# Optimization experiments

Hardware: AMD Instinct MI355X
Metric: run time of the kernel (lower is better)

The kernel has to match this reference:

```python
import math
import jax, jax.numpy as jnp
import numpy as np

NUM_HEADS = 32
HIDDEN = 4096
HEAD_DIM = HIDDEN // NUM_HEADS  # 128
NEG_INF = -1e30


def _alibi_slopes(n: int) -> jnp.ndarray:
    cp2 = 2 ** math.floor(math.log2(n))
    base = 2.0 ** (-(2.0 ** (-(math.log2(cp2) - 3))))
    slopes = base ** np.arange(1, cp2 + 1, dtype=np.float64)
    if cp2 != n:
        extra_base = 2.0 ** (-(2.0 ** (-(math.log2(2 * cp2) - 3))))
        rem = min(cp2, n - cp2)
        extra = extra_base ** np.arange(1, 1 + 2 * rem, 2, dtype=np.float64)
        slopes = np.concatenate([slopes, extra])
    return jnp.asarray(slopes, dtype=jnp.float32)


def setup_inputs() -> dict:
    key = jax.random.key(0)
    k1, k2, k3 = jax.random.split(key, 3)
    B, S = 2, 2048
    hidden_states = jax.random.normal(k1, (B, S, HIDDEN), dtype=jnp.float32)
    Wqkv = jax.random.normal(k2, (HIDDEN, NUM_HEADS * HEAD_DIM + 2 * HEAD_DIM), dtype=jnp.float32) * 0.02
    Wo = jax.random.normal(k3, (HIDDEN, HIDDEN), dtype=jnp.float32) * 0.02
    return {"hidden_states": hidden_states, "Wqkv": Wqkv, "Wo": Wo}


def reference(hidden_states, Wqkv, Wo):
    B, S, H = hidden_states.shape
    nH, d = NUM_HEADS, HEAD_DIM
    scale = d ** -0.5

    qkv = hidden_states @ Wqkv                      # [B,S,nH*d + 2d]
    q = qkv[..., : nH * d].reshape(B, S, nH, d)     # [B,S,nH,d]
    k = qkv[..., nH * d: nH * d + d]                # [B,S,d] (single kv head, MQA)
    v = qkv[..., nH * d + d:]                       # [B,S,d]

    scores = jnp.einsum("bqhd,bkd->bhqk", q, k) * scale  # [B,nH,S,S]

    pos_q = jnp.arange(S)[:, None]
    pos_k = jnp.arange(S)[None, :]
    slopes = _alibi_slopes(nH)                       # [nH]
    alibi = slopes[:, None, None] * (pos_k - pos_q).astype(jnp.float32)  # [nH,S,S]
    causal = pos_k <= pos_q                          # [S,S]

    scores = jnp.where(causal[None, None], scores + alibi[None], NEG_INF)
    probs = jax.nn.softmax(scores, axis=-1)
    attn = jnp.einsum("bhqk,bkd->bqhd", probs, v).reshape(B, S, H)
    return attn @ Wo
```

## Files before the change

kernel.cpp:

```cpp
#include <hip/hip_runtime.h>
#include <hip/hip_bf16.h>

typedef __attribute__((ext_vector_type(8))) short bf16x8;
typedef __attribute__((ext_vector_type(4))) float f32x4;
typedef __attribute__((ext_vector_type(8))) unsigned short u16x8;
typedef __attribute__((ext_vector_type(4))) unsigned short u16x4;

__device__ __forceinline__ unsigned short f2bf(float x) {
    union { float f; unsigned u; } v; v.f = x;
    unsigned r = v.u + 0x7fff + ((v.u >> 16) & 1);
    return (unsigned short)(r >> 16);
}

__device__ __forceinline__ unsigned short f2bf_hw(float x) {
    __hip_bfloat16 h = __float2bfloat16(x);
    return *reinterpret_cast<unsigned short*>(&h);
}

__device__ __forceinline__ void gload16(const void* g, void* l) {
    __builtin_amdgcn_global_load_lds(
        (const __attribute__((address_space(1))) void*)g,
        (__attribute__((address_space(3))) void*)l, 16, 0, 0);
}

__global__ __launch_bounds__(256) void cast_bf16_kernel(
    const float* __restrict__ src, unsigned short* __restrict__ dst, int n8) {
    int i = blockIdx.x * 256 + threadIdx.x;
    if (i >= n8) return;
    const float4* s = (const float4*)src + (size_t)i * 2;
    float4 a = s[0], b = s[1];
    u16x8 o;
    o[0] = f2bf(a.x); o[1] = f2bf(a.y); o[2] = f2bf(a.z); o[3] = f2bf(a.w);
    o[4] = f2bf(b.x); o[5] = f2bf(b.y); o[6] = f2bf(b.z); o[7] = f2bf(b.w);
    *(u16x8*)(dst + (size_t)i * 8) = o;
}

__global__ __launch_bounds__(256) void transpose_cast_kernel(
    const float* __restrict__ src, unsigned short* __restrict__ dst, int R, int C) {
    __shared__ float tile[32][33];
    const int bx = blockIdx.x * 32, by = blockIdx.y * 32;
    const int tx = threadIdx.x & 31, ty = threadIdx.x >> 5;
#pragma unroll
    for (int i = 0; i < 32; i += 8)
        tile[ty + i][tx] = src[(size_t)(by + ty + i) * C + (bx + tx)];
    __syncthreads();
#pragma unroll
    for (int i = 0; i < 32; i += 8)
        dst[(size_t)(bx + ty + i) * R + (by + tx)] = f2bf(tile[tx][ty + i]);
}

template <int OUTBF>
__global__ __launch_bounds__(256) void gemm_kernel(
    const unsigned short* __restrict__ A, const unsigned short* __restrict__ BT,
    void* __restrict__ Cp, int M, int N, int K) {
    __shared__ unsigned short Al[2][128 * 32];
    __shared__ unsigned short Bl[2][128 * 32];
    const int t = threadIdx.x;
    const int wid = t >> 6, lane = t & 63;
    const int l15 = lane & 15, lg = lane >> 4;
    const int bm = blockIdx.y * 128, bn = blockIdx.x * 128;
    const int wm = (wid >> 1) * 64, wn = (wid & 1) * 64;

    f32x4 acc[4][4];
#pragma unroll
    for (int i = 0; i < 4; ++i)
#pragma unroll
        for (int j = 0; j < 4; ++j) acc[i][j] = (f32x4)(0.f);

    const int nk = K >> 5;
    const int c0 = t, c1 = t + 256;

    auto stage = [&](int buf, int kt) {
        const unsigned short* Ab = A + (size_t)bm * K + kt * 32;
        const unsigned short* Bb = BT + (size_t)bn * K + kt * 32;
        gload16(Ab + (size_t)(c0 >> 2) * K + (c0 & 3) * 8, &Al[buf][wid * 64 * 8]);
        gload16(Ab + (size_t)(c1 >> 2) * K + (c1 & 3) * 8, &Al[buf][(256 + wid * 64) * 8]);
        gload16(Bb + (size_t)(c0 >> 2) * K + (c0 & 3) * 8, &Bl[buf][wid * 64 * 8]);
        gload16(Bb + (size_t)(c1 >> 2) * K + (c1 & 3) * 8, &Bl[buf][(256 + wid * 64) * 8]);
    };

    stage(0, 0);
    __syncthreads();
    for (int kt = 0; kt < nk; ++kt) {
        const int cur = kt & 1;
        if (kt + 1 < nk) stage(cur ^ 1, kt + 1);
        bf16x8 af[4], bfr[4];
#pragma unroll
        for (int i = 0; i < 4; ++i) {
            af[i]  = *(const bf16x8*)&Al[cur][(wm + i * 16 + l15) * 32 + lg * 8];
            bfr[i] = *(const bf16x8*)&Bl[cur][(wn + i * 16 + l15) * 32 + lg * 8];
        }
#pragma unroll
        for (int i = 0; i < 4; ++i)
#pragma unroll
            for (int j = 0; j < 4; ++j)
                acc[i][j] = __builtin_amdgcn_mfma_f32_16x16x32_bf16(af[i], bfr[j], acc[i][j], 0, 0, 0);
        __syncthreads();
    }

#pragma unroll
    for (int i = 0; i < 4; ++i)
#pragma unroll
        for (int j = 0; j < 4; ++j)
#pragma unroll
            for (int r = 0; r < 4; ++r) {
                const int row = bm + wm + i * 16 + lg * 4 + r;
                const int col = bn + wn + j * 16 + l15;
                if (OUTBF) ((unsigned short*)Cp)[(size_t)row * N + col] = f2bf(acc[i][j][r]);
                else       ((float*)Cp)[(size_t)row * N + col] = acc[i][j][r];
            }
}

#define SYNC1() do { __builtin_amdgcn_s_barrier(); \
    asm volatile("s_waitcnt lgkmcnt(0)" ::: "memory"); } while (0)
#define GATE6() do { asm volatile("s_waitcnt vmcnt(6)" ::: "memory"); \
    __builtin_amdgcn_s_barrier(); __builtin_amdgcn_sched_barrier(0); } while (0)

template <int OUTBF>
__global__ __launch_bounds__(512, 2) void gemm256_kernel(
    const unsigned short* __restrict__ A, const unsigned short* __restrict__ BT,
    void* __restrict__ Cp, int K, int N) {
    __shared__ __align__(16) char lds[131072];
    const int t = threadIdx.x;
    const int wid = t >> 6, lane = t & 63;
    const int l15 = lane & 15, lg = lane >> 4;
    const int xcd = blockIdx.x & 7, idx = blockIdx.x >> 3;
    const int bm = ((xcd >> 1) * 4 + (idx >> 3)) * 256;
    const int bn = ((xcd & 1) * 8 + (idx & 7)) * 256;
    const int wmh = wid >> 2;
    const int wq  = wid & 3;
    const int bhf = wq >> 1;
    const int br0 = (wq & 1) * 64;

    auto Ab = [&](int b, int h) -> char* { return lds + ((b * 2 + h) << 14); };
    auto Bb = [&](int b, int h) -> char* { return lds + 65536 + ((b * 2 + h) << 14); };

    auto stage = [&](char* halfBase, const unsigned short* mat, int rowBase, int kt) {
#pragma unroll
        for (int j = 0; j < 2; ++j) {
            const int dbase = ((j << 3) + wid) << 10;
            const int q = (dbase + lane * 16) ^ (lane & 32);
            const int p = q >> 13, r = (q >> 6) & 127, cb = q & 63;
            gload16(mat + (size_t)(rowBase + r) * K + (kt << 6) + (p << 5) + (cb >> 1),
                    halfBase + dbase);
        }
    };

    f32x4 acc[8][4];
#pragma unroll
    for (int i = 0; i < 8; ++i)
#pragma unroll
        for (int j = 0; j < 4; ++j) acc[i][j] = (f32x4)(0.f);

    bf16x8 af[8][2];
    bf16x8 bfr[2][2];

    auto ldA = [&](int b) {
        const char* base = Ab(b, wmh);
#pragma unroll
        for (int i = 0; i < 8; ++i) {
            const int r = i * 16 + l15;
            const int sw = ((r >> 3) & 1) << 5;
#pragma unroll
            for (int kk = 0; kk < 2; ++kk)
                af[i][kk] = *(const bf16x8*)(base + ((kk * 8192 + r * 64 + lg * 16) ^ sw));
        }
    };
    auto ldB = [&](int b, int nh) {
        const char* base = Bb(b, bhf);
#pragma unroll
        for (int i = 0; i < 2; ++i) {
            const int r = br0 + (nh * 2 + i) * 16 + l15;
            const int sw = ((r >> 3) & 1) << 5;
#pragma unroll
            for (int kk = 0; kk < 2; ++kk)
                bfr[i][kk] = *(const bf16x8*)(base + ((kk * 8192 + r * 64 + lg * 16) ^ sw));
        }
    };
    auto MF = [&](int mh, int nh) {
        __builtin_amdgcn_s_setprio(1);
#pragma unroll
        for (int i = 0; i < 4; ++i)
#pragma unroll
            for (int j = 0; j < 2; ++j)
#pragma unroll
                for (int kk = 0; kk < 2; ++kk)
                    acc[mh * 4 + i][nh * 2 + j] = __builtin_amdgcn_mfma_f32_16x16x32_bf16(
                        af[mh * 4 + i][kk], bfr[j][kk], acc[mh * 4 + i][nh * 2 + j], 0, 0, 0);
        __builtin_amdgcn_s_setprio(0);
    };

    stage(Ab(0, 0), A, bm, 0);
    stage(Ab(0, 1), A, bm + 128, 0);
    stage(Bb(0, 0), BT, bn, 0);
    stage(Bb(0, 1), BT, bn + 128, 0);
    stage(Ab(1, 0), A, bm, 1);
    stage(Ab(1, 1), A, bm + 128, 1);
    stage(Bb(1, 0), BT, bn, 1);
    asm volatile("s_waitcnt vmcnt(6)" ::: "memory");
    __builtin_amdgcn_s_barrier();
    __builtin_amdgcn_sched_barrier(0);

    const int kmask = (K >> 6) - 1;
    const int niter = K >> 7;
    for (int it = 0; it < niter; ++it) {
        const int kto = 2 * it + 1;
        const int kne = (2 * it + 2) & kmask;
        const int kno = (2 * it + 3) & kmask;
        ldA(0); ldB(0, 0);
        stage(Bb(1, 1), BT, bn + 128, kto);
        SYNC1(); MF(0, 0); __builtin_amdgcn_s_barrier();
        stage(Ab(0, 0), A, bm, kne);
        SYNC1(); MF(1, 0); __builtin_amdgcn_s_barrier();
        ldB(0, 1);
        stage(Ab(0, 1), A, bm + 128, kne);
        SYNC1(); MF(1, 1); __builtin_amdgcn_s_barrier();
        stage(Bb(0, 0), BT, bn, kne);
        SYNC1(); MF(0, 1); GATE6();
        ldA(1); ldB(1, 0);
        stage(Bb(0, 1), BT, bn + 128, kne);
        SYNC1(); MF(0, 0); __builtin_amdgcn_s_barrier();
        stage(Ab(1, 0), A, bm, kno);
        SYNC1(); MF(1, 0); __builtin_amdgcn_s_barrier();
        ldB(1, 1);
        stage(Ab(1, 1), A, bm + 128, kno);
        SYNC1(); MF(1, 1); __builtin_amdgcn_s_barrier();
        stage(Bb(1, 0), BT, bn, kno);
        SYNC1(); MF(0, 1); GATE6();
    }

#pragma unroll
    for (int mi = 0; mi < 8; ++mi)
#pragma unroll
        for (int ni = 0; ni < 4; ++ni)
#pragma unroll
            for (int rr = 0; rr < 4; ++rr) {
                const size_t off = (size_t)(bm + wmh * 128 + mi * 16 + lg * 4 + rr) * N +
                                   bn + wq * 64 + ni * 16 + l15;
                if (OUTBF) ((unsigned short*)Cp)[off] = f2bf(acc[mi][ni][rr]);
                else       ((float*)Cp)[off] = acc[mi][ni][rr];
            }
}

__global__ __launch_bounds__(256, 4) void attn_kernel(
    const unsigned short* __restrict__ qkv, unsigned short* __restrict__ attn, int S) {
    constexpr int LD = 4352;
    __shared__ unsigned short Kl[64 * 128];
    __shared__ unsigned short Vt[128 * 64];
    __shared__ unsigned short Pl[4][16 * 64];
    const int t = threadIdx.x, wid = t >> 6;
    const int lane = t & 63, l15 = lane & 15, lg = lane >> 4;
    const int h = blockIdx.y, b = blockIdx.z;
    const size_t rb = (size_t)b * S;
    const int nQB = S >> 6;
    const float scale2 = 0.08838834764831845f * 1.4426950408889634f;
    const float slope2 = exp2f(-0.25f * (float)(h + 1)) * 1.4426950408889634f;
    const float sr1 = slope2, sr2 = slope2 * 2.f, sr3 = slope2 * 3.f;

    for (int half = 0; half < 2; ++half) {
        const int qblk = half ? (nQB - 1 - (int)blockIdx.x) : (int)blockIdx.x;
        const int q0w = qblk * 64 + wid * 16;
        const int qlane = q0w + l15;
        const float aq = slope2 * (float)qlane;

        bf16x8 qf[4];
        {
            const unsigned short* qrow = qkv + (rb + qlane) * LD + h * 128 + lg * 8;
#pragma unroll
            for (int j = 0; j < 4; ++j) qf[j] = *(const bf16x8*)(qrow + j * 32);
        }
        f32x4 o[8];
#pragma unroll
        for (int i = 0; i < 8; ++i) o[i] = (f32x4)(0.f);
        float m_ = -1e30f, l_ = 0.f;

        const int ntile = qblk + 1;
        for (int tile = 0; tile < ntile; ++tile) {
            const int t0 = tile * 64;
            {
                const char* kbase = (const char*)(qkv + (rb + t0) * LD + 4096);
#pragma unroll
                for (int i = 0; i < 4; ++i) {
                    const int c = i * 256 + t;
                    const int krow = c >> 4;
                    gload16(kbase + (size_t)krow * (LD * 2) + (((c & 15) * 16) ^ ((krow & 7) << 4)),
                            (char*)Kl + (i * 256 + wid * 64) * 16);
                }
            }
            {
                const unsigned short* vs = qkv + (rb + t0 + lane) * LD + 4224 + wid * 32;
                u16x8 v0 = *(const u16x8*)vs;
                u16x8 v1 = *(const u16x8*)(vs + 8);
                u16x8 v2 = *(const u16x8*)(vs + 16);
                u16x8 v3 = *(const u16x8*)(vs + 24);
                const int kb = 2 * lane;
#pragma unroll
                for (int e = 0; e < 8; ++e) {
                    int dd = wid * 32 + e;
                    *(unsigned short*)((char*)Vt + dd * 128 + (kb ^ ((dd & 7) << 4))) = v0[e];
                    dd += 8;
                    *(unsigned short*)((char*)Vt + dd * 128 + (kb ^ ((dd & 7) << 4))) = v1[e];
                    dd += 8;
                    *(unsigned short*)((char*)Vt + dd * 128 + (kb ^ ((dd & 7) << 4))) = v2[e];
                    dd += 8;
                    *(unsigned short*)((char*)Vt + dd * 128 + (kb ^ ((dd & 7) << 4))) = v3[e];
                }
            }
            __syncthreads();

            f32x4 s4[4];
#pragma unroll
            for (int ct = 0; ct < 4; ++ct) {
                s4[ct] = (f32x4)(0.f);
                const int row = ct * 16 + l15;
                const int swz = (row & 7) << 4;
#pragma unroll
                for (int j = 0; j < 4; ++j) {
                    bf16x8 kf = *(const bf16x8*)((const char*)Kl + row * 256 +
                                                 ((j * 64 + lg * 16) ^ swz));
                    s4[ct] = __builtin_amdgcn_mfma_f32_16x16x32_bf16(kf, qf[j], s4[ct], 0, 0, 0);
                }
            }

            const float base = slope2 * (float)(t0 + lg * 4) - aq;
            float p4[4][4];
            float mx = -1e30f;
            const bool lastt = (tile == ntile - 1);
            const int dbase = t0 + lg * 4 - qlane;
#pragma unroll
            for (int ct = 0; ct < 4; ++ct) {
                const float bbc = base + slope2 * 16.f * (float)ct;
#pragma unroll
                for (int r = 0; r < 4; ++r) {
                    float sc = fmaf(s4[ct][r], scale2,
                                    bbc + (r == 0 ? 0.f : (r == 1 ? sr1 : (r == 2 ? sr2 : sr3))));
                    if (lastt && (dbase + ct * 16 + r > 0)) sc = -1e30f;
                    p4[ct][r] = sc;
                    mx = fmaxf(mx, sc);
                }
            }
            mx = fmaxf(mx, __shfl_xor(mx, 16));
            mx = fmaxf(mx, __shfl_xor(mx, 32));

            if (!__all(mx <= m_ + 8.0f)) {
                const float mnew = fmaxf(m_, mx);
                const float corr = exp2f(m_ - mnew);
                m_ = mnew;
                l_ *= corr;
                float cr[4];
#pragma unroll
                for (int r = 0; r < 4; ++r) cr[r] = __shfl(corr, lg * 4 + r);
#pragma unroll
                for (int n = 0; n < 8; ++n) {
                    o[n][0] *= cr[0]; o[n][1] *= cr[1];
                    o[n][2] *= cr[2]; o[n][3] *= cr[3];
                }
            }

            float rs = 0.f;
#pragma unroll
            for (int ct = 0; ct < 4; ++ct)
#pragma unroll
                for (int r = 0; r < 4; ++r) {
                    const float pv = exp2f(p4[ct][r] - m_);
                    p4[ct][r] = pv;
                    rs += pv;
                }
            rs += __shfl_xor(rs, 16);
            rs += __shfl_xor(rs, 32);
            l_ += rs;

            {
                char* pb = (char*)&Pl[wid][0] + l15 * 128;
                const int swz = (l15 & 7) << 4;
#pragma unroll
                for (int ct = 0; ct < 4; ++ct) {
                    u16x4 w;
                    w[0] = f2bf_hw(p4[ct][0]); w[1] = f2bf_hw(p4[ct][1]);
                    w[2] = f2bf_hw(p4[ct][2]); w[3] = f2bf_hw(p4[ct][3]);
                    *(u16x4*)(pb + ((ct * 32 + lg * 8) ^ swz)) = w;
                }
            }

            const char* pb = (const char*)&Pl[wid][0] + l15 * 128;
            const int pswz = (l15 & 7) << 4;
            bf16x8 pa0 = *(const bf16x8*)(pb + ((lg * 16) ^ pswz));
            bf16x8 pa1 = *(const bf16x8*)(pb + ((64 + lg * 16) ^ pswz));
#pragma unroll
            for (int n = 0; n < 8; ++n) {
                const int dd = n * 16 + l15;
                const int vswz = (dd & 7) << 4;
                bf16x8 vf0 = *(const bf16x8*)((const char*)Vt + dd * 128 + ((lg * 16) ^ vswz));
                bf16x8 vf1 = *(const bf16x8*)((const char*)Vt + dd * 128 + ((64 + lg * 16) ^ vswz));
                f32x4 a4 = __builtin_amdgcn_mfma_f32_16x16x32_bf16(pa0, vf0, o[n], 0, 0, 0);
                o[n] = __builtin_amdgcn_mfma_f32_16x16x32_bf16(pa1, vf1, a4, 0, 0, 0);
            }
            __syncthreads();
        }

        const float rl = 1.f / l_;
        float rv[4];
#pragma unroll
        for (int r = 0; r < 4; ++r) rv[r] = __shfl(rl, lg * 4 + r);
#pragma unroll
        for (int n = 0; n < 8; ++n)
#pragma unroll
            for (int r = 0; r < 4; ++r) {
                const int q = q0w + lg * 4 + r;
                attn[(rb + q) * 4096 + h * 128 + n * 16 + l15] = f2bf(o[n][r] * rv[r]);
            }
    }
}

extern "C" void kernel_launch(void* const* d_in, const int* in_sizes, int n_in,
                              void* d_out, int out_size, void* d_ws, size_t ws_size,
                              hipStream_t stream) {
    const float* hidden = (const float*)d_in[0];
    const float* Wqkv   = (const float*)d_in[1];
    const float* Wo     = (const float*)d_in[2];
    float* out = (float*)d_out;
    char* ws = (char*)d_ws;

    const int B = 2, S = 2048, H = 4096, NQ = 4352;
    const int M = B * S;

    unsigned short* hb  = (unsigned short*)(ws);
    unsigned short* wT  = (unsigned short*)(ws + 33554432);
    unsigned short* qkv = (unsigned short*)(ws + 33554432 + 35651584);

    cast_bf16_kernel<<<(M * H / 8) / 256, 256, 0, stream>>>(hidden, hb, M * H / 8);
    transpose_cast_kernel<<<dim3(NQ / 32, H / 32), 256, 0, stream>>>(Wqkv, wT, H, NQ);
    gemm_kernel<1><<<dim3(NQ / 128, M / 128), 256, 0, stream>>>(hb, wT, qkv, M, NQ, H);
    transpose_cast_kernel<<<dim3(H / 32, H / 32), 256, 0, stream>>>(Wo, wT, H, H);
    attn_kernel<<<dim3(16, 32, 2), 256, 0, stream>>>(qkv, hb, S);
    gemm256_kernel<0><<<dim3(256), 512, 0, stream>>>(hb, wT, out, H, H);
}
```

Before: 554.9 us.

## Load A fragments per quarter and double-buffer B fragments in gemm256 pipeline

The 256x256 GEMM main loop now keeps only half of the A fragments in registers (4 row tiles instead of 8) and alternates between two B fragment buffers. The MFMA quadrant order becomes a snake pattern (00,01,11,10) so loaded fragments are reused across consecutive quadrants. The global-to-LDS staging order and prologue change accordingly, and the vmcnt gate drops from 6 to 4. The goal is lower VGPR pressure and better overlap of LDS reads with MFMA work. The cost is extra LDS fragment reloads and a riskier hazard ordering between staged buffers and reads.

```diff
diff --git a/kernel.cpp b/kernel.cpp
--- a/kernel.cpp
+++ b/kernel.cpp
@@ -113,7 +113,7 @@
 
 #define SYNC1() do { __builtin_amdgcn_s_barrier(); \
     asm volatile("s_waitcnt lgkmcnt(0)" ::: "memory"); } while (0)
-#define GATE6() do { asm volatile("s_waitcnt vmcnt(6)" ::: "memory"); \
+#define GATE4() do { asm volatile("s_waitcnt vmcnt(4)" ::: "memory"); \
     __builtin_amdgcn_s_barrier(); __builtin_amdgcn_sched_barrier(0); } while (0)
 
 template <int OUTBF>
@@ -152,21 +152,21 @@
 #pragma unroll
         for (int j = 0; j < 4; ++j) acc[i][j] = (f32x4)(0.f);
 
-    bf16x8 af[8][2];
-    bf16x8 bfr[2][2];
-
-    auto ldA = [&](int b) {
+    bf16x8 afq[4][2];
+    bf16x8 b0[2][2], b1[2][2];
+
+    auto ldAq = [&](int b, int mh) {
         const char* base = Ab(b, wmh);
 #pragma unroll
-        for (int i = 0; i < 8; ++i) {
-            const int r = i * 16 + l15;
+        for (int i = 0; i < 4; ++i) {
+            const int r = mh * 64 + i * 16 + l15;
             const int sw = ((r >> 3) & 1) << 5;
 #pragma unroll
             for (int kk = 0; kk < 2; ++kk)
-                af[i][kk] = *(const bf16x8*)(base + ((kk * 8192 + r * 64 + lg * 16) ^ sw));
+                afq[i][kk] = *(const bf16x8*)(base + ((kk * 8192 + r * 64 + lg * 16) ^ sw));
         }
     };
-    auto ldB = [&](int b, int nh) {
+    auto ldBq = [&](bf16x8 (&bq)[2][2], int b, int nh) {
         const char* base = Bb(b, bhf);
 #pragma unroll
         for (int i = 0; i < 2; ++i) {
@@ -174,10 +174,10 @@
             const int sw = ((r >> 3) & 1) << 5;
 #pragma unroll
             for (int kk = 0; kk < 2; ++kk)
-                bfr[i][kk] = *(const bf16x8*)(base + ((kk * 8192 + r * 64 + lg * 16) ^ sw));
+                bq[i][kk] = *(const bf16x8*)(base + ((kk * 8192 + r * 64 + lg * 16) ^ sw));
         }
     };
-    auto MF = [&](int mh, int nh) {
+    auto MFq = [&](int mh, int nh, bf16x8 (&bq)[2][2]) {
         __builtin_amdgcn_s_setprio(1);
 #pragma unroll
         for (int i = 0; i < 4; ++i)
@@ -186,7 +186,7 @@
 #pragma unroll
                 for (int kk = 0; kk < 2; ++kk)
                     acc[mh * 4 + i][nh * 2 + j] = __builtin_amdgcn_mfma_f32_16x16x32_bf16(
-                        af[mh * 4 + i][kk], bfr[j][kk], acc[mh * 4 + i][nh * 2 + j], 0, 0, 0);
+                        afq[i][kk], bq[j][kk], acc[mh * 4 + i][nh * 2 + j], 0, 0, 0);
         __builtin_amdgcn_s_setprio(0);
     };
 
@@ -194,10 +194,9 @@
     stage(Ab(0, 1), A, bm + 128, 0);
     stage(Bb(0, 0), BT, bn, 0);
     stage(Bb(0, 1), BT, bn + 128, 0);
-    stage(Ab(1, 0), A, bm, 1);
-    stage(Ab(1, 1), A, bm + 128, 1);
     stage(Bb(1, 0), BT, bn, 1);
-    asm volatile("s_waitcnt vmcnt(6)" ::: "memory");
+    stage(Bb(1, 1), BT, bn + 128, 1);
+    asm volatile("s_waitcnt vmcnt(4)" ::: "memory");
     __builtin_amdgcn_s_barrier();
     __builtin_amdgcn_sched_barrier(0);
 
@@ -207,26 +206,28 @@
         const int kto = 2 * it + 1;
         const int kne = (2 * it + 2) & kmask;
         const int kno = (2 * it + 3) & kmask;
-        ldA(0); ldB(0, 0);
-        stage(Bb(1, 1), BT, bn + 128, kto);
-        SYNC1(); MF(0, 0); __builtin_amdgcn_s_barrier();
+        ldAq(0, 0); ldBq(b0, 0, 0);
+        stage(Ab(1, 0), A, bm, kto);
+        SYNC1(); MFq(0, 0, b0); __builtin_amdgcn_s_barrier();
+        ldBq(b1, 0, 1);
+        stage(Ab(1, 1), A, bm + 128, kto);
+        SYNC1(); MFq(0, 1, b1); __builtin_amdgcn_s_barrier();
+        ldAq(0, 1);
+        stage(Bb(0, 0), BT, bn, kne);
+        SYNC1(); MFq(1, 1, b1); __builtin_amdgcn_s_barrier();
+        stage(Bb(0, 1), BT, bn + 128, kne);
+        SYNC1(); MFq(1, 0, b0); GATE4();
+        ldAq(1, 0); ldBq(b0, 1, 0);
         stage(Ab(0, 0), A, bm, kne);
-        SYNC1(); MF(1, 0); __builtin_amdgcn_s_barrier();
-        ldB(0, 1);
+        SYNC1(); MFq(0, 0, b0); __builtin_amdgcn_s_barrier();
+        ldBq(b1, 1, 1);
         stage(Ab(0, 1), A, bm + 128, kne);
-        SYNC1(); MF(1, 1); __builtin_amdgcn_s_barrier();
-        stage(Bb(0, 0), BT, bn, kne);
-        SYNC1(); MF(0, 1); GATE6();
-        ldA(1); ldB(1, 0);
-        stage(Bb(0, 1), BT, bn + 128, kne);
-        SYNC1(); MF(0, 0); __builtin_amdgcn_s_barrier();
-        stage(Ab(1, 0), A, bm, kno);
-        SYNC1(); MF(1, 0); __builtin_amdgcn_s_barrier();
-        ldB(1, 1);
-        stage(Ab(1, 1), A, bm + 128, kno);
-        SYNC1(); MF(1, 1); __builtin_amdgcn_s_barrier();
+        SYNC1(); MFq(0, 1, b1); __builtin_amdgcn_s_barrier();
+        ldAq(1, 1);
         stage(Bb(1, 0), BT, bn, kno);
-        SYNC1(); MF(0, 1); GATE6();
+        SYNC1(); MFq(1, 1, b1); __builtin_amdgcn_s_barrier();
+        stage(Bb(1, 1), BT, bn + 128, kno);
+        SYNC1(); MFq(1, 0, b0); GATE4();
     }
 
 #pragma unroll
```

Measured after the change: 520.9 us. -6.1%, faster.
